# Kernel optimization log

Hardware: AMD Instinct MI355X
Metric: run time of the kernel (lower is better)

The kernel has to match this reference:

```python
import jax, jax.numpy as jnp
import numpy as np

N = 4096
DIM_IN = 512
DIM_Q = 128
DIM_K = 128
NUM_GRAPHS = 16
NODES_PER_GRAPH = N // NUM_GRAPHS
NEG = -1000000.0


def setup_inputs() -> dict:
    key = jax.random.key(0)
    ks = jax.random.split(key, 10)
    x = jax.random.normal(ks[0], (N, DIM_IN), dtype=jnp.float32)
    b = jax.random.normal(ks[1], (N, N), dtype=jnp.float32)
    c = jax.random.normal(ks[2], (N, N), dtype=jnp.float32)
    sparse_mask = jax.random.randint(ks[3], (N, N), 0, 2).astype(jnp.int32)
    ptr = (jnp.arange(NUM_GRAPHS + 1) * NODES_PER_GRAPH).astype(jnp.int32)
    # linear layer params (q, k, v): y = x @ W.T + bias
    Wq = jax.random.normal(ks[4], (DIM_Q, DIM_IN), dtype=jnp.float32) * 0.02
    bq = jnp.zeros((DIM_Q,), dtype=jnp.float32)
    Wk = jax.random.normal(ks[5], (DIM_K, DIM_IN), dtype=jnp.float32) * 0.02
    bk = jnp.zeros((DIM_K,), dtype=jnp.float32)
    Wv = jax.random.normal(ks[6], (DIM_K, DIM_IN), dtype=jnp.float32) * 0.02
    bv = jnp.zeros((DIM_K,), dtype=jnp.float32)
    return {"x": x, "b": b, "c": c, "ptr": ptr, "sparse_mask": sparse_mask,
            "Wq": Wq, "bq": bq, "Wk": Wk, "bk": bk, "Wv": Wv, "bv": bv}


def reference(x, b, c, ptr, sparse_mask, Wq, bq, Wk, bk, Wv, bv):
    n = x.shape[0]
    q = x @ Wq.T + bq            # [N, dq]
    k = x @ Wk.T + bk            # [N, dk]
    v = x @ Wv.T + bv            # [N, dk]
    # graph id per node from ptr; block-diagonal (same-graph) mask
    gid = jnp.searchsorted(ptr, jnp.arange(n), side='right') - 1
    block = gid[:, None] == gid[None, :]                       # [N, N] bool
    scale = q.shape[-1] ** 0.5
    # compute_a: QK^T/sqrt(dq) on the block diagonal, zeros elsewhere
    a = jnp.where(block, (q @ k.T) / scale, 0.0)
    a = a + b + c
    keep = block & (sparse_mask != 0)
    a = jnp.where(keep, a, NEG)
    sm = jax.nn.softmax(a, axis=-1) * keep.astype(x.dtype)
    return sm @ v
```

## Files before the change

### kernel.cpp

```cpp
#include <hip/hip_runtime.h>
#include <hip/hip_bf16.h>

#define N_NODES 4096
#define DIM_IN 512
#define DIM_QK 128
#define BLK 256
#define NUM_G 16
#define NEGV -1000000.0f

typedef __bf16 bf16x8 __attribute__((ext_vector_type(8)));
typedef float  f32x4  __attribute__((ext_vector_type(4)));

__global__ __launch_bounds__(256) void cvt_kernel(
    const float* __restrict__ x,
    const float* __restrict__ Wq, const float* __restrict__ Wk,
    const float* __restrict__ Wv,
    __bf16* __restrict__ xb, __bf16* __restrict__ wb)
{
    const int i = blockIdx.x * 256 + threadIdx.x;
    if (i < 524288) {
        const float4 v = ((const float4*)x)[i];
        __bf16* o = xb + i * 4;
        o[0] = (__bf16)v.x; o[1] = (__bf16)v.y;
        o[2] = (__bf16)v.z; o[3] = (__bf16)v.w;
    } else {
        const int j = i - 524288;
        if (j < 49152) {
            const int m = j / 16384;
            const float* W = (m == 0) ? Wq : (m == 1 ? Wk : Wv);
            const float4 v = ((const float4*)W)[j - m * 16384];
            __bf16* o = wb + j * 4;
            o[0] = (__bf16)v.x; o[1] = (__bf16)v.y;
            o[2] = (__bf16)v.z; o[3] = (__bf16)v.w;
        }
    }
}

__global__ __launch_bounds__(256) void bcm_kernel(
    const float* __restrict__ b, const float* __restrict__ c,
    const int* __restrict__ mask, float* __restrict__ D)
{
    const int i   = blockIdx.x * 256 + threadIdx.x;
    const int g   = i >> 14;
    const int rem = i & 16383;
    const int rA  = rem >> 6;
    const int c4  = rem & 63;
    const size_t src = (size_t)(g * 256 + rA) * N_NODES + g * 256 + c4 * 4;

    const float4 bb = *(const float4*)(b + src);
    const float4 cc = *(const float4*)(c + src);
    const int4   mm = *(const int4*)(mask + src);
    float4 d;
    d.x = mm.x ? bb.x + cc.x : NEGV;
    d.y = mm.y ? bb.y + cc.y : NEGV;
    d.z = mm.z ? bb.z + cc.z : NEGV;
    d.w = mm.w ? bb.w + cc.w : NEGV;

    const int tile = rA >> 4, rl = rA & 15;
    const int quad = rl >> 2, rr = rl & 3;
    const int nt = c4 >> 2, lr0 = (c4 & 3) * 4;
    const int dst = ((((g * 16 + tile) * 16 + nt) * 4 + rr) * 64) + quad * 16 + lr0;
    *(float4*)(D + dst) = d;
}

__global__ __launch_bounds__(256) void qkv_mfma(
    const __bf16* __restrict__ xb, const __bf16* __restrict__ wb,
    const float* __restrict__ bq, const float* __restrict__ bk,
    const float* __restrict__ bv,
    __bf16* __restrict__ qb, __bf16* __restrict__ kb, __bf16* __restrict__ vtb)
{
    const int mat    = blockIdx.y >> 1;
    const int colOff = (blockIdx.y & 1) * 64;
    const int wave = threadIdx.x >> 6;
    const int lane = threadIdx.x & 63;
    const int lr   = lane & 15;
    const int quad = lane >> 4;
    const int row0 = blockIdx.x * 64 + wave * 16;

    const __bf16* W    = wb + mat * (DIM_QK * DIM_IN);
    const float*  bias = (mat == 0) ? bq : (mat == 1 ? bk : bv);

    f32x4 acc[4];
    #pragma unroll
    for (int i = 0; i < 4; ++i) acc[i] = (f32x4){0.f, 0.f, 0.f, 0.f};

    const __bf16* arow = xb + (size_t)(row0 + lr) * DIM_IN + quad * 8;
    const __bf16* brow = W + (size_t)(colOff + lr) * DIM_IN + quad * 8;

    #pragma unroll 4
    for (int kt = 0; kt < 16; ++kt) {
        const bf16x8 a = *(const bf16x8*)(arow + kt * 32);
        #pragma unroll
        for (int nt = 0; nt < 4; ++nt) {
            const bf16x8 b = *(const bf16x8*)(brow + nt * 16 * DIM_IN + kt * 32);
            acc[nt] = __builtin_amdgcn_mfma_f32_16x16x32_bf16(a, b, acc[nt], 0, 0, 0);
        }
    }

    #pragma unroll
    for (int nt = 0; nt < 4; ++nt) {
        const int col = colOff + nt * 16 + lr;
        const float bs = bias[col];
        #pragma unroll
        for (int r = 0; r < 4; ++r) {
            const int row = row0 + quad * 4 + r;
            const __bf16 o = (__bf16)(acc[nt][r] + bs);
            if (mat == 0)      qb[(size_t)row * DIM_QK + col] = o;
            else if (mat == 1) kb[(size_t)row * DIM_QK + col] = o;
            else               vtb[(size_t)col * N_NODES + row] = o;
        }
    }
}

#define PSTR 272

__global__ __launch_bounds__(256) void attn_mfma(
    const float* __restrict__ D,
    const __bf16* __restrict__ qb, const __bf16* __restrict__ kb,
    const __bf16* __restrict__ vtb,
    float* __restrict__ out)
{
    __shared__ __bf16 plds[16 * PSTR];
    __shared__ float redm[4][16];
    __shared__ float reds[4][16];

    const int tid  = threadIdx.x;
    const int w    = tid >> 6;
    const int lane = tid & 63;
    const int lr   = lane & 15;
    const int quad = lane >> 4;
    const int g    = blockIdx.x >> 4;
    const int tile = blockIdx.x & 15;
    const int row0 = g * BLK + tile * 16;
    const int col0 = g * BLK;

    bf16x8 aq[4];
    #pragma unroll
    for (int kt = 0; kt < 4; ++kt)
        aq[kt] = *(const bf16x8*)(qb + (size_t)(row0 + lr) * DIM_QK + kt * 32 + quad * 8);

    f32x4 s[4];
    #pragma unroll
    for (int nt = 0; nt < 4; ++nt) s[nt] = (f32x4){0.f, 0.f, 0.f, 0.f};

    #pragma unroll
    for (int kt = 0; kt < 4; ++kt) {
        #pragma unroll
        for (int nt = 0; nt < 4; ++nt) {
            const bf16x8 b = *(const bf16x8*)(kb
                + (size_t)(col0 + w * 64 + nt * 16 + lr) * DIM_QK + kt * 32 + quad * 8);
            s[nt] = __builtin_amdgcn_mfma_f32_16x16x32_bf16(aq[kt], b, s[nt], 0, 0, 0);
        }
    }

    const float rscale = 0.08838834764831845f;
    const float* Dg = D + (size_t)(((g * 16 + tile) * 16 + w * 4) * 4) * 64;
    #pragma unroll
    for (int nt = 0; nt < 4; ++nt)
        #pragma unroll
        for (int r = 0; r < 4; ++r)
            s[nt][r] = s[nt][r] * rscale + Dg[(nt * 4 + r) * 64 + lane];

    float mr[4] = {-3e38f, -3e38f, -3e38f, -3e38f};
    #pragma unroll
    for (int nt = 0; nt < 4; ++nt)
        #pragma unroll
        for (int r = 0; r < 4; ++r) mr[r] = fmaxf(mr[r], s[nt][r]);
    #pragma unroll
    for (int off = 1; off <= 8; off <<= 1)
        #pragma unroll
        for (int r = 0; r < 4; ++r) mr[r] = fmaxf(mr[r], __shfl_xor(mr[r], off));
    if (lr == 0) {
        #pragma unroll
        for (int r = 0; r < 4; ++r) redm[w][quad * 4 + r] = mr[r];
    }
    __syncthreads();
    float M[4];
    #pragma unroll
    for (int r = 0; r < 4; ++r) {
        const int rw = quad * 4 + r;
        M[r] = fmaxf(fmaxf(redm[0][rw], redm[1][rw]), fmaxf(redm[2][rw], redm[3][rw]));
    }

    float sum[4] = {0.f, 0.f, 0.f, 0.f};
    #pragma unroll
    for (int nt = 0; nt < 4; ++nt)
        #pragma unroll
        for (int r = 0; r < 4; ++r) {
            const float e = (s[nt][r] > -1e5f) ? __expf(s[nt][r] - M[r]) : 0.f;
            s[nt][r] = e;
            sum[r] += e;
        }
    #pragma unroll
    for (int off = 1; off <= 8; off <<= 1)
        #pragma unroll
        for (int r = 0; r < 4; ++r) sum[r] += __shfl_xor(sum[r], off);
    if (lr == 0) {
        #pragma unroll
        for (int r = 0; r < 4; ++r) reds[w][quad * 4 + r] = sum[r];
    }
    __syncthreads();
    float inv[4];
    #pragma unroll
    for (int r = 0; r < 4; ++r) {
        const int rw = quad * 4 + r;
        const float t = reds[0][rw] + reds[1][rw] + reds[2][rw] + reds[3][rw];
        inv[r] = (t > 0.f) ? (1.f / t) : 0.f;
    }

    #pragma unroll
    for (int nt = 0; nt < 4; ++nt)
        #pragma unroll
        for (int r = 0; r < 4; ++r)
            plds[(quad * 4 + r) * PSTR + w * 64 + nt * 16 + lr] =
                (__bf16)(s[nt][r] * inv[r]);
    __syncthreads();

    #pragma unroll
    for (int nt2 = 0; nt2 < 2; ++nt2) {
        f32x4 o = (f32x4){0.f, 0.f, 0.f, 0.f};
        #pragma unroll
        for (int kt = 0; kt < 8; ++kt) {
            const bf16x8 a = *(const bf16x8*)(plds + lr * PSTR + kt * 32 + quad * 8);
            const bf16x8 b = *(const bf16x8*)(vtb
                + (size_t)(w * 32 + nt2 * 16 + lr) * N_NODES + col0 + kt * 32 + quad * 8);
            o = __builtin_amdgcn_mfma_f32_16x16x32_bf16(a, b, o, 0, 0, 0);
        }
        #pragma unroll
        for (int r = 0; r < 4; ++r)
            out[(size_t)(row0 + quad * 4 + r) * DIM_QK + w * 32 + nt2 * 16 + lr] = o[r];
    }
}

extern "C" void kernel_launch(void* const* d_in, const int* in_sizes, int n_in,
                              void* d_out, int out_size, void* d_ws, size_t ws_size,
                              hipStream_t stream) {
    const float* x    = (const float*)d_in[0];
    const float* bmat = (const float*)d_in[1];
    const float* cmat = (const float*)d_in[2];
    const int*   mask = (const int*)d_in[4];
    const float* Wq   = (const float*)d_in[5];
    const float* bq   = (const float*)d_in[6];
    const float* Wk   = (const float*)d_in[7];
    const float* bk   = (const float*)d_in[8];
    const float* Wv   = (const float*)d_in[9];
    const float* bv   = (const float*)d_in[10];
    float* out = (float*)d_out;

    __bf16* xb  = (__bf16*)d_ws;
    __bf16* wb  = xb + (size_t)N_NODES * DIM_IN;
    __bf16* qb  = wb + 3 * DIM_QK * DIM_IN;
    __bf16* kb  = qb + (size_t)N_NODES * DIM_QK;
    __bf16* vtb = kb + (size_t)N_NODES * DIM_QK;
    float*  Dp  = (float*)(vtb + (size_t)DIM_QK * N_NODES);

    cvt_kernel<<<dim3((524288 + 49152 + 255) / 256), 256, 0, stream>>>(
        x, Wq, Wk, Wv, xb, wb);

    bcm_kernel<<<dim3(1024), 256, 0, stream>>>(bmat, cmat, mask, Dp);

    qkv_mfma<<<dim3(N_NODES / 64, 6), 256, 0, stream>>>(
        xb, wb, bq, bk, bv, qb, kb, vtb);

    attn_mfma<<<dim3(NUM_G * 16), 256, 0, stream>>>(Dp, qb, kb, vtb, out);
}
```

Before: 203.7 us.

## Fuse b+c+mask preprocessing into attention kernel and prefetch K/V into registers

New measurement: 196.4 us. 1.04x faster.

```diff
diff --git a/kernel.cpp b/kernel.cpp
--- a/kernel.cpp
+++ b/kernel.cpp
@@ -36,34 +36,7 @@
     }
 }
 
-__global__ __launch_bounds__(256) void bcm_kernel(
-    const float* __restrict__ b, const float* __restrict__ c,
-    const int* __restrict__ mask, float* __restrict__ D)
-{
-    const int i   = blockIdx.x * 256 + threadIdx.x;
-    const int g   = i >> 14;
-    const int rem = i & 16383;
-    const int rA  = rem >> 6;
-    const int c4  = rem & 63;
-    const size_t src = (size_t)(g * 256 + rA) * N_NODES + g * 256 + c4 * 4;
-
-    const float4 bb = *(const float4*)(b + src);
-    const float4 cc = *(const float4*)(c + src);
-    const int4   mm = *(const int4*)(mask + src);
-    float4 d;
-    d.x = mm.x ? bb.x + cc.x : NEGV;
-    d.y = mm.y ? bb.y + cc.y : NEGV;
-    d.z = mm.z ? bb.z + cc.z : NEGV;
-    d.w = mm.w ? bb.w + cc.w : NEGV;
-
-    const int tile = rA >> 4, rl = rA & 15;
-    const int quad = rl >> 2, rr = rl & 3;
-    const int nt = c4 >> 2, lr0 = (c4 & 3) * 4;
-    const int dst = ((((g * 16 + tile) * 16 + nt) * 4 + rr) * 64) + quad * 16 + lr0;
-    *(float4*)(D + dst) = d;
-}
-
-__global__ __launch_bounds__(256) void qkv_mfma(
+__global__ __launch_bounds__(128) void qkv_mfma(
     const __bf16* __restrict__ xb, const __bf16* __restrict__ wb,
     const float* __restrict__ bq, const float* __restrict__ bk,
     const float* __restrict__ bv,
@@ -75,7 +48,7 @@
     const int lane = threadIdx.x & 63;
     const int lr   = lane & 15;
     const int quad = lane >> 4;
-    const int row0 = blockIdx.x * 64 + wave * 16;
+    const int row0 = blockIdx.x * 32 + wave * 16;
 
     const __bf16* W    = wb + mat * (DIM_QK * DIM_IN);
     const float*  bias = (mat == 0) ? bq : (mat == 1 ? bk : bv);
@@ -114,8 +87,9 @@
 
 #define PSTR 272
 
-__global__ __launch_bounds__(256) void attn_mfma(
-    const float* __restrict__ D,
+__global__ __launch_bounds__(256, 1) void attn_mfma(
+    const float* __restrict__ bmat, const float* __restrict__ cmat,
+    const int* __restrict__ mask,
     const __bf16* __restrict__ qb, const __bf16* __restrict__ kb,
     const __bf16* __restrict__ vtb,
     float* __restrict__ out)
@@ -139,27 +113,54 @@
     for (int kt = 0; kt < 4; ++kt)
         aq[kt] = *(const bf16x8*)(qb + (size_t)(row0 + lr) * DIM_QK + kt * 32 + quad * 8);
 
+    bf16x8 bk[16];
+    #pragma unroll
+    for (int kt = 0; kt < 4; ++kt)
+        #pragma unroll
+        for (int nt = 0; nt < 4; ++nt)
+            bk[kt * 4 + nt] = *(const bf16x8*)(kb
+                + (size_t)(col0 + w * 64 + nt * 16 + lr) * DIM_QK + kt * 32 + quad * 8);
+
+    bf16x8 bv[16];
+    #pragma unroll
+    for (int nt2 = 0; nt2 < 2; ++nt2)
+        #pragma unroll
+        for (int kt = 0; kt < 8; ++kt)
+            bv[nt2 * 8 + kt] = *(const bf16x8*)(vtb
+                + (size_t)(w * 32 + nt2 * 16 + lr) * N_NODES + col0 + kt * 32 + quad * 8);
+
+    float bbv[16], ccv[16];
+    int   mmv[16];
+    #pragma unroll
+    for (int nt = 0; nt < 4; ++nt)
+        #pragma unroll
+        for (int r = 0; r < 4; ++r) {
+            const size_t idx = (size_t)(row0 + quad * 4 + r) * N_NODES
+                             + col0 + w * 64 + nt * 16 + lr;
+            bbv[nt * 4 + r] = bmat[idx];
+            ccv[nt * 4 + r] = cmat[idx];
+            mmv[nt * 4 + r] = mask[idx];
+        }
+
     f32x4 s[4];
     #pragma unroll
     for (int nt = 0; nt < 4; ++nt) s[nt] = (f32x4){0.f, 0.f, 0.f, 0.f};
 
     #pragma unroll
-    for (int kt = 0; kt < 4; ++kt) {
-        #pragma unroll
-        for (int nt = 0; nt < 4; ++nt) {
-            const bf16x8 b = *(const bf16x8*)(kb
-                + (size_t)(col0 + w * 64 + nt * 16 + lr) * DIM_QK + kt * 32 + quad * 8);
-            s[nt] = __builtin_amdgcn_mfma_f32_16x16x32_bf16(aq[kt], b, s[nt], 0, 0, 0);
-        }
-    }
+    for (int kt = 0; kt < 4; ++kt)
+        #pragma unroll
+        for (int nt = 0; nt < 4; ++nt)
+            s[nt] = __builtin_amdgcn_mfma_f32_16x16x32_bf16(aq[kt], bk[kt * 4 + nt],
+                                                            s[nt], 0, 0, 0);
 
     const float rscale = 0.08838834764831845f;
-    const float* Dg = D + (size_t)(((g * 16 + tile) * 16 + w * 4) * 4) * 64;
-    #pragma unroll
-    for (int nt = 0; nt < 4; ++nt)
-        #pragma unroll
-        for (int r = 0; r < 4; ++r)
-            s[nt][r] = s[nt][r] * rscale + Dg[(nt * 4 + r) * 64 + lane];
+    #pragma unroll
+    for (int nt = 0; nt < 4; ++nt)
+        #pragma unroll
+        for (int r = 0; r < 4; ++r) {
+            const int i = nt * 4 + r;
+            s[nt][r] = mmv[i] ? (s[nt][r] * rscale + bbv[i] + ccv[i]) : NEGV;
+        }
 
     float mr[4] = {-3e38f, -3e38f, -3e38f, -3e38f};
     #pragma unroll
@@ -222,9 +223,7 @@
         #pragma unroll
         for (int kt = 0; kt < 8; ++kt) {
             const bf16x8 a = *(const bf16x8*)(plds + lr * PSTR + kt * 32 + quad * 8);
-            const bf16x8 b = *(const bf16x8*)(vtb
-                + (size_t)(w * 32 + nt2 * 16 + lr) * N_NODES + col0 + kt * 32 + quad * 8);
-            o = __builtin_amdgcn_mfma_f32_16x16x32_bf16(a, b, o, 0, 0, 0);
+            o = __builtin_amdgcn_mfma_f32_16x16x32_bf16(a, bv[nt2 * 8 + kt], o, 0, 0, 0);
         }
         #pragma unroll
         for (int r = 0; r < 4; ++r)
@@ -252,15 +251,13 @@
     __bf16* qb  = wb + 3 * DIM_QK * DIM_IN;
     __bf16* kb  = qb + (size_t)N_NODES * DIM_QK;
     __bf16* vtb = kb + (size_t)N_NODES * DIM_QK;
-    float*  Dp  = (float*)(vtb + (size_t)DIM_QK * N_NODES);
 
     cvt_kernel<<<dim3((524288 + 49152 + 255) / 256), 256, 0, stream>>>(
         x, Wq, Wk, Wv, xb, wb);
 
-    bcm_kernel<<<dim3(1024), 256, 0, stream>>>(bmat, cmat, mask, Dp);
-
-    qkv_mfma<<<dim3(N_NODES / 64, 6), 256, 0, stream>>>(
+    qkv_mfma<<<dim3(128, 6), 128, 0, stream>>>(
         xb, wb, bq, bk, bv, qb, kb, vtb);
 
-    attn_mfma<<<dim3(NUM_G * 16), 256, 0, stream>>>(Dp, qb, kb, vtb, out);
-}
+    attn_mfma<<<dim3(NUM_G * 16), 256, 0, stream>>>(
+        bmat, cmat, mask, qb, kb, vtb, out);
+}
```
